# Optimization experiments

Measured on AMD Instinct MI355X. Metric: run time of the kernel, lower is better.

The kernel has to match this reference:

```python
import jax, jax.numpy as jnp
import numpy as np
import math

EPS = 1e-5
N_HEADS = 4


def _ln(x, g, b):
    mu = jnp.mean(x, axis=-1, keepdims=True)
    var = jnp.mean((x - mu) ** 2, axis=-1, keepdims=True)
    return (x - mu) * jax.lax.rsqrt(var + EPS) * g + b


def _eq_ln(s, v, g, b, vscale):
    # scalar LayerNorm + equivariant vector norm rescaling
    s = _ln(s, g, b)
    vn = jnp.sqrt(jnp.sum(v * v, axis=-1, keepdims=True))  # (B,N,C,1)
    v = v / (vn + EPS) * jnp.mean(vn, axis=-2, keepdims=True) * vscale[None, None, :, None]
    return s, v


def _block(s, v, pos, Wq, bq, Wk, bk, Wv, bv, Wo, bo, w_dist, b_dist, Wvv, Wvo,
           g1, be1, vs1, g2, be2, vs2, Wf1, bf1, Wf2, bf2, Wfv1, Wfv2):
    B, N, S = s.shape
    D = S // N_HEADS
    # --- norm1 + attention ---
    sn, vn = _eq_ln(s, v, g1, be1, vs1)
    q = (sn @ Wq + bq).reshape(B, N, N_HEADS, D)
    k = (sn @ Wk + bk).reshape(B, N, N_HEADS, D)
    vs = (sn @ Wv + bv).reshape(B, N, N_HEADS, D)
    attn = jnp.einsum('bnhd,bmhd->bhnm', q, k) / math.sqrt(D)
    # pairwise Euclidean distance via the |x|^2 + |y|^2 - 2xy trick (clamped for sqrt safety)
    p2 = jnp.sum(pos * pos, axis=-1)  # (B,N)
    d2 = p2[:, :, None] + p2[:, None, :] - 2.0 * jnp.einsum('bnd,bmd->bnm', pos, pos)
    dist = jnp.sqrt(jnp.maximum(d2, 1e-12))  # (B,N,N)
    # dist_proj: Linear(1 -> n_heads) + Softplus, applied per pair
    bias = jax.nn.softplus(dist[..., None] * w_dist + b_dist)  # (B,N,N,H)
    attn = jax.nn.softmax(attn - jnp.transpose(bias, (0, 3, 1, 2)), axis=-1)  # (B,H,N,N)
    attn_mean = jnp.mean(attn, axis=1)  # (B,N,N)
    s_attn = jnp.einsum('bhnm,bmhd->bnhd', attn, vs).reshape(B, N, S) @ Wo + bo
    # vector channel mixing + rotation by head-averaged attention
    v_mix = jnp.einsum('bncx,ce->bnex', vn, Wvv)          # (B,N,C,3)
    v_attn = jnp.einsum('bnm,bmcx->bncx', attn_mean, v_mix)
    v_attn = jnp.einsum('bncx,ce->bnex', v_attn, Wvo)
    s = s + s_attn
    v = v + v_attn
    # --- norm2 + FFN ---
    sn, vn = _eq_ln(s, v, g2, be2, vs2)
    s = s + (jax.nn.gelu(sn @ Wf1 + bf1, approximate=False) @ Wf2 + bf2)
    v = v + jnp.einsum('bnhx,hc->bncx', jnp.einsum('bncx,ch->bnhx', vn, Wfv1), Wfv2)
    return s, v


def setup_inputs() -> dict:
    B, N, S, C, H = 4, 2048, 256, 64, N_HEADS
    key = jax.random.key(0)
    ks = jax.random.split(key, 24)

    def nrm(k, shape, scale=0.02):
        return jax.random.normal(k, shape, dtype=jnp.float32) * scale

    return {
        's': jax.random.normal(ks[0], (B, N, S), dtype=jnp.float32),
        'v': jax.random.normal(ks[1], (B, N, C, 3), dtype=jnp.float32),
        'pos': jax.random.normal(ks[2], (B, N, 3), dtype=jnp.float32),
        'Wq': nrm(ks[3], (S, S)), 'bq': nrm(ks[4], (S,)),
        'Wk': nrm(ks[5], (S, S)), 'bk': nrm(ks[6], (S,)),
        'Wv': nrm(ks[7], (S, S)), 'bv': nrm(ks[8], (S,)),
        'Wo': nrm(ks[9], (S, S)), 'bo': nrm(ks[10], (S,)),
        'w_dist': nrm(ks[11], (H,), 0.5), 'b_dist': nrm(ks[12], (H,), 0.5),
        'Wvv': nrm(ks[13], (C, C)), 'Wvo': nrm(ks[14], (C, C)),
        'g1': jnp.ones((S,), jnp.float32), 'be1': jnp.zeros((S,), jnp.float32),
        'vs1': jnp.ones((C,), jnp.float32),
        'g2': jnp.ones((S,), jnp.float32), 'be2': jnp.zeros((S,), jnp.float32),
        'vs2': jnp.ones((C,), jnp.float32),
        'Wf1': nrm(ks[15], (S, 4 * S)), 'bf1': nrm(ks[16], (4 * S,)),
        'Wf2': nrm(ks[17], (4 * S, S)), 'bf2': nrm(ks[18], (S,)),
        'Wfv1': nrm(ks[19], (C, 4 * C)), 'Wfv2': nrm(ks[20], (4 * C, C)),
    }


def reference(s, v, pos, Wq, bq, Wk, bk, Wv, bv, Wo, bo, w_dist, b_dist, Wvv, Wvo,
              g1, be1, vs1, g2, be2, vs2, Wf1, bf1, Wf2, bf2, Wfv1, Wfv2):
    return _block(s, v, pos, Wq, bq, Wk, bk, Wv, bv, Wo, bo, w_dist, b_dist, Wvv, Wvo,
                  g1, be1, vs1, g2, be2, vs2, Wf1, bf1, Wf2, bf2, Wfv1, Wfv2)
```

## Files before the change

### kernel.cpp

```cpp
#include <hip/hip_runtime.h>
#include <hip/hip_bf16.h>

using bf16 = __hip_bfloat16;
typedef __attribute__((ext_vector_type(8))) short short8;
typedef __attribute__((ext_vector_type(4))) float float4v;
typedef __attribute__((ext_vector_type(16))) float f32x16;
typedef __attribute__((ext_vector_type(4))) unsigned uint4v;

__device__ __forceinline__ float b2f(bf16 x){ return __bfloat162float(x); }
__device__ __forceinline__ bf16  f2b(float x){ return __float2bfloat16(x); }
__device__ __forceinline__ bf16  tob(float x){ return f2b(x); }
__device__ __forceinline__ bf16  tob(bf16 x){ return x; }
__device__ __forceinline__ float frcp(float x){ return __builtin_amdgcn_rcpf(x); }
__device__ __forceinline__ float bs2f(short s){
  unsigned u = ((unsigned)(unsigned short)s) << 16;
  return __builtin_bit_cast(float, u);
}
__device__ __forceinline__ unsigned cvt_pk_bf16(float lo, float hi){
  unsigned r; asm("v_cvt_pk_bf16_f32 %0, %1, %2" : "=v"(r) : "v"(lo), "v"(hi)); return r;
}
__device__ __forceinline__ void plswap(unsigned &a, unsigned &b){
  asm("v_permlane32_swap_b32 %0, %1" : "+v"(a), "+v"(b));
}

#define EPSV 1e-5f
#define Z16 {0.f,0.f,0.f,0.f,0.f,0.f,0.f,0.f,0.f,0.f,0.f,0.f,0.f,0.f,0.f,0.f}

__global__ __launch_bounds__(256) void pos_kernel(const float* __restrict__ pos,
                                                  float* __restrict__ posf, int rows){
  int r = blockIdx.x*256 + threadIdx.x;
  if (r >= rows) return;
  float x = pos[3*r], y = pos[3*r+1], z = pos[3*r+2];
  posf[4*r] = x; posf[4*r+1] = y; posf[4*r+2] = z; posf[4*r+3] = x*x + y*y + z*z;
}

struct WTDesc { const float* src; bf16* dst; int rows, cols; };
struct WTPack { WTDesc d[10]; };

__global__ __launch_bounds__(256) void wtrans_kernel(WTPack p){
  WTDesc w = p.d[blockIdx.z];
  long r0 = (long)blockIdx.y*32, c0 = (long)blockIdx.x*32;
  if (r0 >= w.rows || c0 >= w.cols) return;
  __shared__ bf16 tile[32][33];
  int tx = threadIdx.x & 31, ty = threadIdx.x >> 5;
#pragma unroll
  for (int i = ty; i < 32; i += 8) tile[i][tx] = f2b(w.src[(r0+i)*w.cols + c0 + tx]);
  __syncthreads();
#pragma unroll
  for (int i = ty; i < 32; i += 8) w.dst[(c0+i)*w.rows + r0 + tx] = tile[tx][i];
}

template<typename TI>
__global__ __launch_bounds__(256) void transpose_kernel(
    const TI* __restrict__ in, long ldin, long is1, long is2,
    bf16* __restrict__ out, long ldout, long os1, long os2, int Z2)
{
  int z = blockIdx.z, z1 = z / Z2, z2 = z - z1*Z2;
  in  += (long)z1*is1 + (long)z2*is2;
  out += (long)z1*os1 + (long)z2*os2;
  __shared__ bf16 tile[32][33];
  int tx = threadIdx.x & 31, ty = threadIdx.x >> 5;
  long r0 = (long)blockIdx.y*32, c0 = (long)blockIdx.x*32;
#pragma unroll
  for (int i = ty; i < 32; i += 8) tile[i][tx] = tob(in[(r0+i)*ldin + c0 + tx]);
  __syncthreads();
#pragma unroll
  for (int i = ty; i < 32; i += 8) out[(c0+i)*ldout + r0 + tx] = tile[tx][i];
}

__global__ __launch_bounds__(256) void bcat_kernel(const float* __restrict__ bq,
                                                   const float* __restrict__ bk,
                                                   const float* __restrict__ bv,
                                                   float* __restrict__ bqkv,
                                                   float* __restrict__ kmax){
  int j = blockIdx.x*256 + threadIdx.x;
  if (blockIdx.x == 0 && threadIdx.x < 16) kmax[threadIdx.x] = 0.f;
  if (j >= 768) return;
  bqkv[j] = (j < 256) ? bq[j] : (j < 512) ? bk[j-256] : bv[j-512];
}

__global__ __launch_bounds__(256) void ln_kernel(const float* __restrict__ x,
                                                 const float* __restrict__ g,
                                                 const float* __restrict__ be,
                                                 bf16* __restrict__ out){
  const long row = blockIdx.x;
  const int t = threadIdx.x, lane = t & 63, wv = t >> 6;
  __shared__ float ws1[4], ws2[4];
  float v = x[(row<<8) + t];
  float s1 = v, s2 = v*v;
#pragma unroll
  for (int off=32; off; off>>=1){
    s1 += __shfl_xor(s1, off);
    s2 += __shfl_xor(s2, off);
  }
  if (lane == 0){ ws1[wv] = s1; ws2[wv] = s2; }
  __syncthreads();
  const float r1 = ws1[0]+ws1[1]+ws1[2]+ws1[3];
  const float r2 = ws2[0]+ws2[1]+ws2[2]+ws2[3];
  const float mu = r1 * (1.f/256.f);
  const float var = r2 * (1.f/256.f) - mu*mu;
  const float rstd = rsqrtf(fmaxf(var, 0.f) + EPSV);
  out[(row<<8)+t] = f2b((v-mu)*rstd*g[t] + be[t]);
}

__global__ __launch_bounds__(192) void vnorm1_kernel(const float* __restrict__ vin,
                                                     const float* __restrict__ vs1,
                                                     bf16* __restrict__ vnX){
  const long row = blockIdx.x;
  const int t = threadIdx.x;
  __shared__ float vv[192], nrm[64];
  __shared__ float smean;
  vv[t] = vin[row*192 + t];
  __syncthreads();
  if (t < 64){
    float a = vv[3*t], b = vv[3*t+1], c = vv[3*t+2];
    float nv = sqrtf(a*a + b*b + c*c);
    nrm[t] = nv;
    float s = nv;
#pragma unroll
    for (int off=32; off; off>>=1) s += __shfl_xor(s, off);
    if (t == 0) smean = s*(1.f/64.f);
  }
  __syncthreads();
  const int c = t/3, x = t - 3*c;
  const float val = vv[t] / (nrm[c] + EPSV) * smean * vs1[c];
  vnX[row*192 + x*64 + c] = f2b(val);
}

__global__ __launch_bounds__(192) void vnorm2_kernel(const float* __restrict__ v2X,
                                                     const float* __restrict__ vs2,
                                                     bf16* __restrict__ vn2X){
  const long row = blockIdx.x;
  const int t = threadIdx.x;
  __shared__ float vv[192], nrm[64];
  __shared__ float smean;
  vv[t] = v2X[row*192 + t];
  __syncthreads();
  if (t < 64){
    float a = vv[t], b = vv[t+64], c = vv[t+128];
    float nv = sqrtf(a*a + b*b + c*c);
    nrm[t] = nv;
    float s = nv;
#pragma unroll
    for (int off=32; off; off>>=1) s += __shfl_xor(s, off);
    if (t == 0) smean = s*(1.f/64.f);
  }
  __syncthreads();
  const int c = t & 63;
  vn2X[row*192 + t] = f2b(vv[t] / (nrm[c] + EPSV) * smean * vs2[c]);
}

__global__ __launch_bounds__(256) void knorm_kernel(const bf16* __restrict__ qkv,
                                                    float* __restrict__ kmax){
  const int bh = blockIdx.x, b = bh>>2, h = bh&3;
  const int t = threadIdx.x, lane = t & 63, wv = t >> 6;
  __shared__ float red[4];
  long row = (long)b*2048 + (long)blockIdx.y*256 + t;
  const short8* kp = (const short8*)(qkv + row*768 + 256 + h*64);
  float ss = 0.f;
#pragma unroll
  for (int c=0;c<8;c++){
    short8 v = kp[c];
#pragma unroll
    for (int j=0;j<8;j++){ float f = bs2f(v[j]); ss = fmaf(f,f,ss); }
  }
#pragma unroll
  for (int off=32; off; off>>=1) ss = fmaxf(ss, __shfl_xor(ss, off));
  if (lane == 0) red[wv] = ss;
  __syncthreads();
  if (t == 0){
    float m = fmaxf(fmaxf(red[0],red[1]), fmaxf(red[2],red[3]));
    atomicMax((unsigned*)&kmax[bh], __float_as_uint(m));
  }
}

#define ATT_K_OFF   0
#define ATT_V_OFF   4096
#define ATT_X_OFF   9216
#define ATT_P_OFF   24576
#define ATT_TILE    25088
#define ATT_GRP     50176
#define ATT_LACC    98304
#define ATT_SMEM    100352

__global__ __launch_bounds__(512, 2) void attn_kernel(
    const bf16* __restrict__ qkv,
    const bf16* __restrict__ vsT,
    const bf16* __restrict__ vmixT,
    const float* __restrict__ posf,
    const float* __restrict__ kmaxA,
    const float* __restrict__ w_dist, const float* __restrict__ b_dist,
    bf16* __restrict__ sA,
    bf16* __restrict__ slab)
{
  __shared__ __align__(16) char smem[ATT_SMEM];
  const int qb = blockIdx.x;
  const int bh = blockIdx.y;
  const int b  = bh >> 2, h = bh & 3;
  const int tid = threadIdx.x;
  const int w = tid >> 6, lane = tid & 63;
  const int g = w >> 2, qw = w & 3;
  const int lq = lane & 31, hi = lane >> 5;
  const int gtid = tid & 255;

  const int qloc = qb*128 + qw*32 + lq;
  const long rowQ = (long)b*2048 + qloc;

  short8 qf[4];
  {
    const bf16* qp = qkv + rowQ*768 + h*64 + hi*8;
#pragma unroll
    for (int kc=0;kc<4;kc++) qf[kc] = *(const short8*)(qp + kc*16);
  }
  float q2 = 0.f;
#pragma unroll
  for (int kc=0;kc<4;kc++)
#pragma unroll
    for (int j=0;j<8;j++){ float qv = bs2f(qf[kc][j]); q2 = fmaf(qv,qv,q2); }
  q2 += __shfl_xor(q2, 32);
  const float mxs = sqrtf(q2 * kmaxA[bh]) * 0.125f;
  const float wh = w_dist[h], bhd = b_dist[h];
  const float4v pn = *(const float4v*)(posf + (long)b*8192 + (long)qloc*4);
  const float m2x = -2.f*pn[0], m2y = -2.f*pn[1], m2z = -2.f*pn[2], pnw = pn[3];

  f32x16 O[2]  = {Z16, Z16};
  f32x16 VM[6] = {Z16, Z16, Z16, Z16, Z16, Z16};
  float lacc = 0.f;

  short8 stK, stV, stX0, stX1, stX2; float4v stP;
  const int sm = gtid >> 3, sc = gtid & 7;
  const int vd = gtid >> 2, vc = gtid & 3;
  const bf16* Kg = qkv + (long)b*2048*768 + 256 + h*64;
  const bf16* Vg = vsT + (long)b*524288 + (long)h*131072;
  const bf16* Xg = vmixT + (long)b*393216;
  const float* Pg = posf + (long)b*8192;
  char* gbase = smem + g*ATT_GRP;

  auto LOADT = [&](int m0){
    stK  = *(const short8*)(Kg + (long)(m0+sm)*768 + sc*8);
    stV  = *(const short8*)(Vg + (long)vd*2048 + m0 + vc*8);
    stX0 = *(const short8*)(Xg + (long)vd*2048 + m0 + vc*8);
    stX1 = *(const short8*)(Xg + (long)(64+vd)*2048 + m0 + vc*8);
    stX2 = *(const short8*)(Xg + (long)(128+vd)*2048 + m0 + vc*8);
    if (gtid < 32) stP = *(const float4v*)(Pg + (long)(m0+gtid)*4);
  };
  auto WRITET = [&](char* buf){
    *(short8*)(buf + ATT_K_OFF + sm*128 + ((sc ^ (sm&7))<<4)) = stK;
    *(short8*)(buf + ATT_V_OFF + vd*80 + vc*16) = stV;
    *(short8*)(buf + ATT_X_OFF + vd*80 + vc*16) = stX0;
    *(short8*)(buf + ATT_X_OFF + (64+vd)*80 + vc*16) = stX1;
    *(short8*)(buf + ATT_X_OFF + (128+vd)*80 + vc*16) = stX2;
    if (gtid < 32) *(float4v*)(buf + ATT_P_OFF + gtid*16) = stP;
  };

  auto COMPUTE = [&](const char* buf){
    const char* Kb = buf + ATT_K_OFF;
    const char* Vb = buf + ATT_V_OFF;
    const char* Xb = buf + ATT_X_OFF;
    const float4v* pmb = (const float4v*)(buf + ATT_P_OFF);
    f32x16 S = Z16;
#pragma unroll
    for (int kc=0;kc<4;kc++){
      short8 kf = *(const short8*)(Kb + lq*128 + (((kc*2+hi) ^ (lq&7))<<4));
      S = __builtin_amdgcn_mfma_f32_32x32x16_bf16(kf, qf[kc], S, 0, 0, 0);
    }
    float P[16];
#pragma unroll
    for (int gg=0; gg<4; gg++){
#pragma unroll
      for (int i=0;i<4;i++){
        float4v pm = pmb[gg*8 + hi*4 + i];
        float d2 = fmaf(m2x, pm[0], fmaf(m2y, pm[1], fmaf(m2z, pm[2], pnw + pm[3])));
        float dist = sqrtf(fmaxf(d2, 1e-12f));
        float sig = frcp(1.f + __expf(fmaf(dist, wh, bhd)));
        float p = __expf(fmaf(S[gg*4+i], 0.125f, -mxs)) * sig;
        lacc += p;
        P[gg*4+i] = p;
      }
    }
    unsigned pk[8];
#pragma unroll
    for (int t=0;t<8;t++) pk[t] = cvt_pk_bf16(P[2*t], P[2*t+1]);
    plswap(pk[0], pk[2]); plswap(pk[1], pk[3]);
    plswap(pk[4], pk[6]); plswap(pk[5], pk[7]);
    uint4v y0v = {pk[0], pk[1], pk[2], pk[3]};
    uint4v y1v = {pk[4], pk[5], pk[6], pk[7]};
    short8 Y0 = __builtin_bit_cast(short8, y0v);
    short8 Y1 = __builtin_bit_cast(short8, y1v);
#pragma unroll
    for (int dblk=0; dblk<2; dblk++){
      short8 v0 = *(const short8*)(Vb + (dblk*32+lq)*80 + hi*16);
      short8 v1 = *(const short8*)(Vb + (dblk*32+lq)*80 + 32 + hi*16);
      O[dblk] = __builtin_amdgcn_mfma_f32_32x32x16_bf16(v0, Y0, O[dblk], 0,0,0);
      O[dblk] = __builtin_amdgcn_mfma_f32_32x32x16_bf16(v1, Y1, O[dblk], 0,0,0);
    }
#pragma unroll
    for (int eblk=0; eblk<6; eblk++){
      short8 x0 = *(const short8*)(Xb + (eblk*32+lq)*80 + hi*16);
      short8 x1 = *(const short8*)(Xb + (eblk*32+lq)*80 + 32 + hi*16);
      VM[eblk] = __builtin_amdgcn_mfma_f32_32x32x16_bf16(x0, Y0, VM[eblk], 0,0,0);
      VM[eblk] = __builtin_amdgcn_mfma_f32_32x32x16_bf16(x1, Y1, VM[eblk], 0,0,0);
    }
  };

  LOADT(g*32);
  WRITET(gbase);
  __syncthreads();
#pragma unroll 1
  for (int i=0; i<32; ++i){
    if (i < 31) LOADT((2*(i+1)+g)*32);
    COMPUTE(gbase + (i&1)*ATT_TILE);
    if (i < 31) WRITET(gbase + ((i+1)&1)*ATT_TILE);
    __syncthreads();
  }

  float* laccT = (float*)(smem + ATT_LACC);
  laccT[w*64 + lane] = lacc;
  if (g == 1){
    float* Od = (float*)(smem + ATT_GRP) + (qw*64+lane)*33;
#pragma unroll
    for (int r=0;r<16;r++){ Od[r] = O[0][r]; Od[16+r] = O[1][r]; }
  }
  __syncthreads();
  const float lsum = laccT[qw*64+lq] + laccT[qw*64+32+lq]
                   + laccT[(4+qw)*64+lq] + laccT[(4+qw)*64+32+lq];
  if (g == 0){
    const float* Od = (const float*)(smem + ATT_GRP) + (qw*64+lane)*33;
#pragma unroll
    for (int r=0;r<16;r++){ O[0][r] += Od[r]; O[1][r] += Od[16+r]; }
  }
  __syncthreads();
#pragma unroll
  for (int hf=0; hf<2; hf++){
    if (g == 0){
      float* Vd = (float*)smem + (qw*64+lane)*49;
#pragma unroll
      for (int e=0;e<3;e++)
#pragma unroll
        for (int r=0;r<16;r++) Vd[e*16+r] = VM[hf*3+e][r];
    }
    __syncthreads();
    if (g == 1){
      const float* Vd = (const float*)smem + (qw*64+lane)*49;
#pragma unroll
      for (int e=0;e<3;e++)
#pragma unroll
        for (int r=0;r<16;r++) VM[hf*3+e][r] += Vd[e*16+r];
    }
    __syncthreads();
  }

  const float sinv = frcp(lsum);
  if (g == 0){
    char* scr = smem + qw*12544;
#pragma unroll
    for (int dblk=0; dblk<2; dblk++)
#pragma unroll
      for (int pp=0; pp<8; pp++){
        const int r = 2*pp;
        const int d = dblk*32 + (r&3) + 8*(r>>2) + 4*hi;
        unsigned u = cvt_pk_bf16(O[dblk][r]*sinv, O[dblk][r+1]*sinv);
        *(unsigned*)(scr + lq*136 + d*2) = u;
      }
  } else {
    const float vinv = 0.25f * sinv;
    char* scr = smem + ATT_GRP + qw*12544;
#pragma unroll
    for (int eblk=0; eblk<6; eblk++)
#pragma unroll
      for (int pp=0; pp<8; pp++){
        const int r = 2*pp;
        const int e = eblk*32 + (r&3) + 8*(r>>2) + 4*hi;
        unsigned u = cvt_pk_bf16(VM[eblk][r]*vinv, VM[eblk][r+1]*vinv);
        *(unsigned*)(scr + lq*392 + e*2) = u;
      }
  }
  __syncthreads();
  if (g == 0){
    const char* scr = smem + qw*12544;
    const int q = lane >> 1, half = lane & 1;
    const char* src = scr + q*136 + half*64;
    char* dst = (char*)(sA + (long)(b*2048 + qb*128 + qw*32 + q)*256 + h*64 + half*32);
#pragma unroll
    for (int i=0;i<8;i++)
      *(unsigned long long*)(dst + i*8) = *(const unsigned long long*)(src + i*8);
  } else {
    const char* scr = smem + ATT_GRP + qw*12544;
    const int q = lane >> 1, half = lane & 1;
    const char* src = scr + q*392 + half*192;
    char* dst = (char*)(slab + (long)h*1572864
                        + (long)(b*2048 + qb*128 + qw*32 + q)*192 + half*96);
#pragma unroll
    for (int i=0;i<24;i++)
      *(unsigned long long*)(dst + i*8) = *(const unsigned long long*)(src + i*8);
  }
}

__global__ __launch_bounds__(256) void hred_kernel(const bf16* __restrict__ slab,
                                                   bf16* __restrict__ out){
  long i = (long)blockIdx.x*256 + threadIdx.x;
  if (i >= 196608) return;
  const short8* s0 = (const short8*)slab + i;
  short8 a = s0[0], b = s0[196608], c = s0[2*196608], d = s0[3*196608];
  short8 o;
#pragma unroll
  for (int j=0;j<8;j++){
    float f = bs2f(a[j]) + bs2f(b[j]) + bs2f(c[j]) + bs2f(d[j]);
    bf16 hv = f2b(f); o[j] = *(short*)&hv;
  }
  ((short8*)out)[i] = o;
}

template<int ACT, int OUTM>
__global__ __launch_bounds__(256) void tgemm64_kernel(
    const bf16* __restrict__ A, long lda,
    const bf16* __restrict__ BT, long ldb,
    const float* __restrict__ bias,
    const float* __restrict__ resid,
    void* __restrict__ Cv, long ldc,
    int K)
{
  __shared__ __align__(16) bf16 As[2][64*32];
  __shared__ __align__(16) bf16 Bs[2][128*32];
  const int tid = threadIdx.x;
  const int wc = tid >> 6, lane = tid & 63;
  const int col = lane & 15, quad = lane >> 4;
  const long rowA0 = (long)blockIdx.y*64;
  const long colB0 = (long)blockIdx.x*128;

  const int tr = tid >> 2, tc = tid & 3;
  const bf16* Ag = A + (rowA0 + tr)*lda + tc*8;
  const bf16* Bg = BT + (colB0 + tr)*ldb + tc*8;

  short8 sa, sb[2];
  auto LOAD = [&](int k0){
    sa = *(const short8*)(Ag + k0);
    sb[0] = *(const short8*)(Bg + k0);
    sb[1] = *(const short8*)(Bg + (long)64*ldb + k0);
  };
  auto STORE = [&](int buf){
    *(short8*)(&As[buf][tr*32 + tc*8]) = sa;
    *(short8*)(&Bs[buf][tr*32 + tc*8]) = sb[0];
    *(short8*)(&Bs[buf][(tr+64)*32 + tc*8]) = sb[1];
  };

  float4v acc[4][2];
#pragma unroll
  for (int m=0;m<4;m++)
#pragma unroll
    for (int n=0;n<2;n++) acc[m][n] = (float4v){0.f,0.f,0.f,0.f};

  LOAD(0); STORE(0);
  __syncthreads();
  const int nk = K >> 5;
#pragma unroll 1
  for (int ks=0; ks<nk; ++ks){
    if (ks+1 < nk) LOAD((ks+1)*32);
    const bf16* Ab = &As[ks&1][col*32 + quad*8];
    const bf16* Bb = &Bs[ks&1][(wc*32 + col)*32 + quad*8];
    short8 af[4], bfv[2];
#pragma unroll
    for (int m=0;m<4;m++) af[m] = *(const short8*)(Ab + m*16*32);
#pragma unroll
    for (int n=0;n<2;n++) bfv[n] = *(const short8*)(Bb + n*16*32);
#pragma unroll
    for (int m=0;m<4;m++)
#pragma unroll
      for (int n=0;n<2;n++)
        acc[m][n] = __builtin_amdgcn_mfma_f32_16x16x32_bf16(af[m], bfv[n], acc[m][n], 0, 0, 0);
    if (ks+1 < nk) STORE((ks+1)&1);
    __syncthreads();
  }

#pragma unroll
  for (int m=0;m<4;m++){
    const long ci0 = rowA0 + m*16 + quad*4;
#pragma unroll
    for (int n=0;n<2;n++){
      const long cj = colB0 + wc*32 + n*16 + col;
      const float bbias = bias ? bias[cj] : 0.f;
#pragma unroll
      for (int r=0;r<4;r++){
        const long ci = ci0 + r;
        float val = acc[m][n][r] + bbias;
        if (ACT == 1) val = 0.5f*val*(1.f + erff(val*0.70710678118654752f));
        if (resid) val += resid[ci*ldc + cj];
        if (OUTM == 0) ((bf16*)Cv)[ci*ldc + cj] = f2b(val);
        else           ((float*)Cv)[ci*ldc + cj] = val;
      }
    }
  }
}

template<int MT, int NT, int ACT, int OUTM, int RXIL, int CXIL>
__global__ __launch_bounds__(64) void gemm_kernel(
    const bf16* __restrict__ A, long lda, long As1, long As2,
    const bf16* __restrict__ BT, long ldb, long Bs1, long Bs2,
    const float* __restrict__ bias,
    const float* __restrict__ resid, long ldr, long Rs1, long Rs2,
    void* __restrict__ Cv, long ldc, long Cs1, long Cs2,
    int K, int Z2, int KS)
{
  int z = blockIdx.z;
  int zz = z / KS, ks = z - zz*KS;
  int z1 = zz / Z2, z2 = zz - z1*Z2;
  A  += (long)z1*As1 + (long)z2*As2 + (long)ks*K;
  BT += (long)z1*Bs1 + (long)z2*Bs2 + (long)ks*K;
  if (resid) resid += (long)z1*Rs1 + (long)z2*Rs2;
  const long cbase = (long)z1*Cs1 + (long)z2*Cs2;

  const int lane = threadIdx.x;
  const int col = lane & 15, quad = lane >> 4;
  const long rowA0 = (long)blockIdx.y*(16*MT);
  const long colB0 = (long)blockIdx.x*(16*NT);

  float4v acc[MT][NT];
#pragma unroll
  for (int m=0;m<MT;m++)
#pragma unroll
    for (int n=0;n<NT;n++) acc[m][n] = (float4v){0.f,0.f,0.f,0.f};

  const bf16* ap[MT];
  const bf16* bp[NT];
#pragma unroll
  for (int m=0;m<MT;m++) ap[m] = A + (rowA0 + m*16 + col)*lda + quad*8;
#pragma unroll
  for (int n=0;n<NT;n++) bp[n] = BT + (colB0 + n*16 + col)*ldb + quad*8;

  for (int k0 = 0; k0 < K; k0 += 32){
    short8 a[MT], bb[NT];
#pragma unroll
    for (int m=0;m<MT;m++){ a[m] = *(const short8*)ap[m]; ap[m] += 32; }
#pragma unroll
    for (int n=0;n<NT;n++){ bb[n] = *(const short8*)bp[n]; bp[n] += 32; }
#pragma unroll
    for (int m=0;m<MT;m++)
#pragma unroll
      for (int n=0;n<NT;n++)
        acc[m][n] = __builtin_amdgcn_mfma_f32_16x16x32_bf16(a[m], bb[n], acc[m][n], 0, 0, 0);
  }

#pragma unroll
  for (int m=0;m<MT;m++){
    const long ri = rowA0 + m*16 + quad*4;
#pragma unroll
    for (int n=0;n<NT;n++){
      const long cj = colB0 + n*16 + col;
      const float bbias = bias ? bias[cj] : 0.f;
#pragma unroll
      for (int r=0;r<4;r++){
        const long ci = ri + r;
        float val = acc[m][n][r] + bbias;
        if (ACT == 1) val = 0.5f*val*(1.f + erff(val*0.70710678118654752f));
        if (resid){
          const long raddr = RXIL ? ((ci/3)*192 + cj*3 + (ci%3)) : (ci*ldr + cj);
          val += resid[raddr];
        }
        const long caddr = CXIL ? (cbase + (ci/3)*192 + cj*3 + (ci%3))
                                : (cbase + ci*ldc + cj);
        if (OUTM == 0)      ((bf16*)Cv)[caddr] = f2b(val);
        else if (OUTM == 1) ((float*)Cv)[caddr] = val;
        else                unsafeAtomicAdd(&((float*)Cv)[caddr], val);
      }
    }
  }
}

extern "C" void kernel_launch(void* const* d_in, const int* in_sizes, int n_in,
                              void* d_out, int out_size, void* d_ws, size_t ws_size,
                              hipStream_t stream)
{
  const float* s    = (const float*)d_in[0];
  const float* v    = (const float*)d_in[1];
  const float* pos  = (const float*)d_in[2];
  const float* Wq   = (const float*)d_in[3];
  const float* bq   = (const float*)d_in[4];
  const float* Wk   = (const float*)d_in[5];
  const float* bk   = (const float*)d_in[6];
  const float* Wv   = (const float*)d_in[7];
  const float* bv   = (const float*)d_in[8];
  const float* Wo   = (const float*)d_in[9];
  const float* bo   = (const float*)d_in[10];
  const float* w_d  = (const float*)d_in[11];
  const float* b_d  = (const float*)d_in[12];
  const float* Wvv  = (const float*)d_in[13];
  const float* Wvo  = (const float*)d_in[14];
  const float* g1   = (const float*)d_in[15];
  const float* be1  = (const float*)d_in[16];
  const float* vs1  = (const float*)d_in[17];
  const float* g2   = (const float*)d_in[18];
  const float* be2  = (const float*)d_in[19];
  const float* vs2  = (const float*)d_in[20];
  const float* Wf1  = (const float*)d_in[21];
  const float* bf1  = (const float*)d_in[22];
  const float* Wf2  = (const float*)d_in[23];
  const float* bf2  = (const float*)d_in[24];
  const float* Wfv1 = (const float*)d_in[25];
  const float* Wfv2 = (const float*)d_in[26];

  float* outS = (float*)d_out;
  float* outV = outS + (size_t)4*2048*256;

  char* w = (char*)d_ws;
  size_t o = 0;
  auto alloc = [&](size_t bytes)->char* {
    char* p = w + o;
    o = (o + bytes + 255) & ~(size_t)255;
    return p;
  };
  float* posf  = (float*)alloc(131072);
  bf16* WqkvT = (bf16*)alloc(393216);
  bf16* WoT   = (bf16*)alloc(131072);
  bf16* Wf1T  = (bf16*)alloc(524288);
  bf16* Wf2T  = (bf16*)alloc(524288);
  bf16* WvvT  = (bf16*)alloc(8192);
  bf16* WvoT  = (bf16*)alloc(8192);
  bf16* Wfv1T = (bf16*)alloc(32768);
  bf16* Wfv2T = (bf16*)alloc(32768);
  float* bqkv = (float*)alloc(3072);
  float* kmax = (float*)alloc(64);
  bf16* sn    = (bf16*)alloc(4194304);
  bf16* qkv   = (bf16*)alloc(12582912);
  bf16* vsT   = (bf16*)alloc(4194304);
  bf16* sA    = (bf16*)alloc(4194304);
  float* s2   = (float*)alloc(8388608);
  bf16* vnX   = (bf16*)alloc(3145728);
  bf16* vmixX = (bf16*)alloc(3145728);
  bf16* vmixXT= (bf16*)alloc(3145728);
  float* v2X  = (float*)alloc(6291456);
  bf16* slab  = (bf16*)alloc(12582912);
  bf16* h1    = (bf16*)alloc(16777216);
  bf16* vn2X  = vnX;
  bf16* tvXb  = vmixX;
  bf16* hv    = qkv;
  if (o > ws_size) return;

  pos_kernel<<<32, 256, 0, stream>>>(pos, posf, 8192);
  WTPack pk;
  pk.d[0] = {Wq,   WqkvT,          256, 256};
  pk.d[1] = {Wk,   WqkvT + 65536,  256, 256};
  pk.d[2] = {Wv,   WqkvT + 131072, 256, 256};
  pk.d[3] = {Wo,   WoT,            256, 256};
  pk.d[4] = {Wf1,  Wf1T,           256, 1024};
  pk.d[5] = {Wf2,  Wf2T,           1024, 256};
  pk.d[6] = {Wvv,  WvvT,           64, 64};
  pk.d[7] = {Wvo,  WvoT,           64, 64};
  pk.d[8] = {Wfv1, Wfv1T,          64, 256};
  pk.d[9] = {Wfv2, Wfv2T,          256, 64};
  wtrans_kernel<<<dim3(32,32,10), 256, 0, stream>>>(pk);
  bcat_kernel<<<3, 256, 0, stream>>>(bq, bk, bv, bqkv, kmax);

  ln_kernel<<<8192, 256, 0, stream>>>(s, g1, be1, sn);
  vnorm1_kernel<<<8192, 192, 0, stream>>>(v, vs1, vnX);

  gemm_kernel<2,4,0,0,0,0><<<dim3(1,768,1), 64, 0, stream>>>(vnX,64,0,0, WvvT,64,0,0,
      nullptr, nullptr,0,0,0, vmixX,64,0,0, 64, 1, 1);
  transpose_kernel<bf16><<<dim3(6,64,4), 256, 0, stream>>>(vmixX, 192, 393216,0,
      vmixXT, 2048, 393216,0, 1);

  tgemm64_kernel<0,0><<<dim3(6,128), 256, 0, stream>>>(sn,256, WqkvT,256,
      bqkv, nullptr, qkv,768, 256);
  transpose_kernel<bf16><<<dim3(2,64,16), 256, 0, stream>>>(qkv+512, 768, 1572864,64,
      vsT, 2048, 524288,131072, 4);

  knorm_kernel<<<dim3(16,8), 256, 0, stream>>>(qkv, kmax);
  attn_kernel<<<dim3(16,16), 512, 0, stream>>>(qkv, vsT, vmixXT, posf, kmax,
      w_d, b_d, sA, slab);
  hred_kernel<<<768, 256, 0, stream>>>(slab, tvXb);

  tgemm64_kernel<0,1><<<dim3(2,128), 256, 0, stream>>>(sA,256, WoT,256,
      bo, s, s2,256, 256);

  gemm_kernel<2,4,0,1,1,0><<<dim3(1,768,1), 64, 0, stream>>>(tvXb,64,0,0, WvoT,64,0,0,
      nullptr, v,0,0,0, v2X,64,0,0, 64, 1, 1);

  ln_kernel<<<8192, 256, 0, stream>>>(s2, g2, be2, sn);
  tgemm64_kernel<1,0><<<dim3(8,128), 256, 0, stream>>>(sn,256, Wf1T,256,
      bf1, nullptr, h1,1024, 256);
  tgemm64_kernel<0,1><<<dim3(2,128), 256, 0, stream>>>(h1,1024, Wf2T,1024,
      bf2, s2, outS,256, 1024);

  vnorm2_kernel<<<8192, 192, 0, stream>>>(v2X, vs2, vn2X);
  tgemm64_kernel<0,0><<<dim3(2,384), 256, 0, stream>>>(vn2X,64, Wfv1T,64,
      nullptr, nullptr, hv,256, 64);
  gemm_kernel<2,4,0,1,0,1><<<dim3(1,768,1), 64, 0, stream>>>(hv,256,0,0, Wfv2T,256,0,0,
      nullptr, v2X,64,0,0, outV,0,0,0, 256, 1, 1);
}
```

Baseline: 377.7 us.

## Merge small setup kernels, fuse head reduction, split-K output GEMMs with atomics

Folds pos and bias-concat into the weight-transpose launch, merges LN with vector-norm and the V transpose with the key-norm pass, and drops the hred kernel by summing the four head slabs inside the Wvo GEMM's A load. The Wo and Wf2 GEMMs become split-K over two z-slices that atomically add into an output pre-filled with residual plus bias by a new addb kernel. This cuts launch count and raises the block count for the small GEMMs. It adds atomic traffic, nondeterministic summation order, and extra passes over memory for the bias prefill.

```diff
diff --git a/kernel.cpp b/kernel.cpp
--- a/kernel.cpp
+++ b/kernel.cpp
@@ -26,23 +26,32 @@
 #define EPSV 1e-5f
 #define Z16 {0.f,0.f,0.f,0.f,0.f,0.f,0.f,0.f,0.f,0.f,0.f,0.f,0.f,0.f,0.f,0.f}
 
-__global__ __launch_bounds__(256) void pos_kernel(const float* __restrict__ pos,
-                                                  float* __restrict__ posf, int rows){
-  int r = blockIdx.x*256 + threadIdx.x;
-  if (r >= rows) return;
-  float x = pos[3*r], y = pos[3*r+1], z = pos[3*r+2];
-  posf[4*r] = x; posf[4*r+1] = y; posf[4*r+2] = z; posf[4*r+3] = x*x + y*y + z*z;
-}
-
 struct WTDesc { const float* src; bf16* dst; int rows, cols; };
 struct WTPack { WTDesc d[10]; };
 
-__global__ __launch_bounds__(256) void wtrans_kernel(WTPack p){
+__global__ __launch_bounds__(256) void wtrans_kernel(WTPack p,
+    const float* __restrict__ pos, float* __restrict__ posf,
+    const float* __restrict__ bq, const float* __restrict__ bk,
+    const float* __restrict__ bv, float* __restrict__ bqkv,
+    float* __restrict__ kmax){
+  const int t = threadIdx.x;
+  if (blockIdx.z == 10){
+    if (blockIdx.y == 0 && blockIdx.x < 32){
+      int r = blockIdx.x*256 + t;
+      float x = pos[3*r], y = pos[3*r+1], z = pos[3*r+2];
+      posf[4*r] = x; posf[4*r+1] = y; posf[4*r+2] = z; posf[4*r+3] = x*x + y*y + z*z;
+    } else if (blockIdx.y == 1 && blockIdx.x < 3){
+      int j = blockIdx.x*256 + t;
+      if (blockIdx.x == 0 && t < 16) kmax[t] = 0.f;
+      bqkv[j] = (j < 256) ? bq[j] : (j < 512) ? bk[j-256] : bv[j-512];
+    }
+    return;
+  }
   WTDesc w = p.d[blockIdx.z];
   long r0 = (long)blockIdx.y*32, c0 = (long)blockIdx.x*32;
   if (r0 >= w.rows || c0 >= w.cols) return;
   __shared__ bf16 tile[32][33];
-  int tx = threadIdx.x & 31, ty = threadIdx.x >> 5;
+  int tx = t & 31, ty = t >> 5;
 #pragma unroll
   for (int i = ty; i < 32; i += 8) tile[i][tx] = f2b(w.src[(r0+i)*w.cols + c0 + tx]);
   __syncthreads();
@@ -68,110 +77,110 @@
   for (int i = ty; i < 32; i += 8) out[(c0+i)*ldout + r0 + tx] = tile[tx][i];
 }
 
-__global__ __launch_bounds__(256) void bcat_kernel(const float* __restrict__ bq,
-                                                   const float* __restrict__ bk,
-                                                   const float* __restrict__ bv,
-                                                   float* __restrict__ bqkv,
-                                                   float* __restrict__ kmax){
-  int j = blockIdx.x*256 + threadIdx.x;
-  if (blockIdx.x == 0 && threadIdx.x < 16) kmax[threadIdx.x] = 0.f;
-  if (j >= 768) return;
-  bqkv[j] = (j < 256) ? bq[j] : (j < 512) ? bk[j-256] : bv[j-512];
-}
-
-__global__ __launch_bounds__(256) void ln_kernel(const float* __restrict__ x,
-                                                 const float* __restrict__ g,
-                                                 const float* __restrict__ be,
-                                                 bf16* __restrict__ out){
-  const long row = blockIdx.x;
-  const int t = threadIdx.x, lane = t & 63, wv = t >> 6;
-  __shared__ float ws1[4], ws2[4];
-  float v = x[(row<<8) + t];
-  float s1 = v, s2 = v*v;
-#pragma unroll
-  for (int off=32; off; off>>=1){
-    s1 += __shfl_xor(s1, off);
-    s2 += __shfl_xor(s2, off);
-  }
-  if (lane == 0){ ws1[wv] = s1; ws2[wv] = s2; }
-  __syncthreads();
-  const float r1 = ws1[0]+ws1[1]+ws1[2]+ws1[3];
-  const float r2 = ws2[0]+ws2[1]+ws2[2]+ws2[3];
-  const float mu = r1 * (1.f/256.f);
-  const float var = r2 * (1.f/256.f) - mu*mu;
-  const float rstd = rsqrtf(fmaxf(var, 0.f) + EPSV);
-  out[(row<<8)+t] = f2b((v-mu)*rstd*g[t] + be[t]);
-}
-
-__global__ __launch_bounds__(192) void vnorm1_kernel(const float* __restrict__ vin,
-                                                     const float* __restrict__ vs1,
-                                                     bf16* __restrict__ vnX){
-  const long row = blockIdx.x;
+__global__ __launch_bounds__(256) void trk_kernel(const bf16* __restrict__ qkv,
+                                                  bf16* __restrict__ vsT,
+                                                  float* __restrict__ kmax){
   const int t = threadIdx.x;
-  __shared__ float vv[192], nrm[64];
-  __shared__ float smean;
-  vv[t] = vin[row*192 + t];
-  __syncthreads();
-  if (t < 64){
-    float a = vv[3*t], b = vv[3*t+1], c = vv[3*t+2];
-    float nv = sqrtf(a*a + b*b + c*c);
-    nrm[t] = nv;
-    float s = nv;
-#pragma unroll
-    for (int off=32; off; off>>=1) s += __shfl_xor(s, off);
-    if (t == 0) smean = s*(1.f/64.f);
-  }
-  __syncthreads();
-  const int c = t/3, x = t - 3*c;
-  const float val = vv[t] / (nrm[c] + EPSV) * smean * vs1[c];
-  vnX[row*192 + x*64 + c] = f2b(val);
-}
-
-__global__ __launch_bounds__(192) void vnorm2_kernel(const float* __restrict__ v2X,
-                                                     const float* __restrict__ vs2,
-                                                     bf16* __restrict__ vn2X){
-  const long row = blockIdx.x;
+  if (blockIdx.z < 16){
+    int z = blockIdx.z, z1 = z >> 2, z2 = z & 3;
+    const bf16* in = qkv + 512 + (long)z1*1572864 + (long)z2*64;
+    bf16* out = vsT + (long)z1*524288 + (long)z2*131072;
+    __shared__ bf16 tile[32][33];
+    int tx = t & 31, ty = t >> 5;
+    long r0 = (long)blockIdx.y*32, c0 = (long)blockIdx.x*32;
+#pragma unroll
+    for (int i = ty; i < 32; i += 8) tile[i][tx] = in[(r0+i)*768 + c0 + tx];
+    __syncthreads();
+#pragma unroll
+    for (int i = ty; i < 32; i += 8) out[(c0+i)*2048 + r0 + tx] = tile[tx][i];
+  } else {
+    const int idx = blockIdx.y*2 + blockIdx.x;
+    const int bh = idx >> 3, chunk = idx & 7;
+    const int b = bh >> 2, h = bh & 3;
+    const int lane = t & 63, wv = t >> 6;
+    __shared__ float red[4];
+    long row = (long)b*2048 + (long)chunk*256 + t;
+    const short8* kp = (const short8*)(qkv + row*768 + 256 + h*64);
+    float ss = 0.f;
+#pragma unroll
+    for (int c=0;c<8;c++){
+      short8 v = kp[c];
+#pragma unroll
+      for (int j=0;j<8;j++){ float f = bs2f(v[j]); ss = fmaf(f,f,ss); }
+    }
+#pragma unroll
+    for (int off=32; off; off>>=1) ss = fmaxf(ss, __shfl_xor(ss, off));
+    if (lane == 0) red[wv] = ss;
+    __syncthreads();
+    if (t == 0){
+      float m = fmaxf(fmaxf(red[0],red[1]), fmaxf(red[2],red[3]));
+      atomicMax((unsigned*)&kmax[bh], __float_as_uint(m));
+    }
+  }
+}
+
+template<int VN>
+__global__ __launch_bounds__(256) void lnvn_kernel(
+    const float* __restrict__ x, const float* __restrict__ g,
+    const float* __restrict__ be, bf16* __restrict__ outln,
+    const float* __restrict__ vin, const float* __restrict__ vs,
+    bf16* __restrict__ outvn)
+{
   const int t = threadIdx.x;
-  __shared__ float vv[192], nrm[64];
-  __shared__ float smean;
-  vv[t] = v2X[row*192 + t];
-  __syncthreads();
-  if (t < 64){
-    float a = vv[t], b = vv[t+64], c = vv[t+128];
-    float nv = sqrtf(a*a + b*b + c*c);
-    nrm[t] = nv;
-    float s = nv;
-#pragma unroll
-    for (int off=32; off; off>>=1) s += __shfl_xor(s, off);
-    if (t == 0) smean = s*(1.f/64.f);
-  }
-  __syncthreads();
-  const int c = t & 63;
-  vn2X[row*192 + t] = f2b(vv[t] / (nrm[c] + EPSV) * smean * vs2[c]);
-}
-
-__global__ __launch_bounds__(256) void knorm_kernel(const bf16* __restrict__ qkv,
-                                                    float* __restrict__ kmax){
-  const int bh = blockIdx.x, b = bh>>2, h = bh&3;
-  const int t = threadIdx.x, lane = t & 63, wv = t >> 6;
-  __shared__ float red[4];
-  long row = (long)b*2048 + (long)blockIdx.y*256 + t;
-  const short8* kp = (const short8*)(qkv + row*768 + 256 + h*64);
-  float ss = 0.f;
-#pragma unroll
-  for (int c=0;c<8;c++){
-    short8 v = kp[c];
-#pragma unroll
-    for (int j=0;j<8;j++){ float f = bs2f(v[j]); ss = fmaf(f,f,ss); }
-  }
-#pragma unroll
-  for (int off=32; off; off>>=1) ss = fmaxf(ss, __shfl_xor(ss, off));
-  if (lane == 0) red[wv] = ss;
-  __syncthreads();
-  if (t == 0){
-    float m = fmaxf(fmaxf(red[0],red[1]), fmaxf(red[2],red[3]));
-    atomicMax((unsigned*)&kmax[bh], __float_as_uint(m));
-  }
+  if (blockIdx.x < 8192){
+    const long row = blockIdx.x;
+    const int lane = t & 63, wv = t >> 6;
+    __shared__ float ws1[4], ws2[4];
+    float v = x[(row<<8) + t];
+    float s1 = v, s2 = v*v;
+#pragma unroll
+    for (int off=32; off; off>>=1){
+      s1 += __shfl_xor(s1, off);
+      s2 += __shfl_xor(s2, off);
+    }
+    if (lane == 0){ ws1[wv] = s1; ws2[wv] = s2; }
+    __syncthreads();
+    const float r1 = ws1[0]+ws1[1]+ws1[2]+ws1[3];
+    const float r2 = ws2[0]+ws2[1]+ws2[2]+ws2[3];
+    const float mu = r1 * (1.f/256.f);
+    const float var = r2 * (1.f/256.f) - mu*mu;
+    const float rstd = rsqrtf(fmaxf(var, 0.f) + EPSV);
+    outln[(row<<8)+t] = f2b((v-mu)*rstd*g[t] + be[t]);
+  } else {
+    const long row = blockIdx.x - 8192;
+    __shared__ float vv[192], nrm[64];
+    __shared__ float smean;
+    if (t < 192) vv[t] = vin[row*192 + t];
+    __syncthreads();
+    if (t < 64){
+      float a, b, c;
+      if (VN == 1){ a = vv[3*t]; b = vv[3*t+1]; c = vv[3*t+2]; }
+      else        { a = vv[t]; b = vv[t+64]; c = vv[t+128]; }
+      float nv = sqrtf(a*a + b*b + c*c);
+      nrm[t] = nv;
+      float s = nv;
+#pragma unroll
+      for (int off=32; off; off>>=1) s += __shfl_xor(s, off);
+      if (t == 0) smean = s*(1.f/64.f);
+    }
+    __syncthreads();
+    if (t < 192){
+      if (VN == 1){
+        const int c = t/3, xx = t - 3*c;
+        outvn[row*192 + xx*64 + c] = f2b(vv[t] / (nrm[c] + EPSV) * smean * vs[c]);
+      } else {
+        const int c = t & 63;
+        outvn[row*192 + t] = f2b(vv[t] / (nrm[c] + EPSV) * smean * vs[c]);
+      }
+    }
+  }
+}
+
+__global__ __launch_bounds__(256) void addb_kernel(const float* __restrict__ in,
+                                                   const float* __restrict__ bias,
+                                                   float* __restrict__ out){
+  long i = (long)blockIdx.x*256 + threadIdx.x;
+  out[i] = in[i] + bias[threadIdx.x];
 }
 
 #define ATT_K_OFF   0
@@ -396,21 +405,6 @@
   }
 }
 
-__global__ __launch_bounds__(256) void hred_kernel(const bf16* __restrict__ slab,
-                                                   bf16* __restrict__ out){
-  long i = (long)blockIdx.x*256 + threadIdx.x;
-  if (i >= 196608) return;
-  const short8* s0 = (const short8*)slab + i;
-  short8 a = s0[0], b = s0[196608], c = s0[2*196608], d = s0[3*196608];
-  short8 o;
-#pragma unroll
-  for (int j=0;j<8;j++){
-    float f = bs2f(a[j]) + bs2f(b[j]) + bs2f(c[j]) + bs2f(d[j]);
-    bf16 hv = f2b(f); o[j] = *(short*)&hv;
-  }
-  ((short8*)out)[i] = o;
-}
-
 template<int ACT, int OUTM>
 __global__ __launch_bounds__(256) void tgemm64_kernel(
     const bf16* __restrict__ A, long lda,
@@ -427,10 +421,11 @@
   const int col = lane & 15, quad = lane >> 4;
   const long rowA0 = (long)blockIdx.y*64;
   const long colB0 = (long)blockIdx.x*128;
+  const long koff = (long)blockIdx.z*K;
 
   const int tr = tid >> 2, tc = tid & 3;
-  const bf16* Ag = A + (rowA0 + tr)*lda + tc*8;
-  const bf16* Bg = BT + (colB0 + tr)*ldb + tc*8;
+  const bf16* Ag = A + (rowA0 + tr)*lda + koff + tc*8;
+  const bf16* Bg = BT + (colB0 + tr)*ldb + koff + tc*8;
 
   short8 sa, sb[2];
   auto LOAD = [&](int k0){
@@ -485,14 +480,15 @@
         float val = acc[m][n][r] + bbias;
         if (ACT == 1) val = 0.5f*val*(1.f + erff(val*0.70710678118654752f));
         if (resid) val += resid[ci*ldc + cj];
-        if (OUTM == 0) ((bf16*)Cv)[ci*ldc + cj] = f2b(val);
-        else           ((float*)Cv)[ci*ldc + cj] = val;
+        if (OUTM == 0)      ((bf16*)Cv)[ci*ldc + cj] = f2b(val);
+        else if (OUTM == 1) ((float*)Cv)[ci*ldc + cj] = val;
+        else                unsafeAtomicAdd(&((float*)Cv)[ci*ldc + cj], val);
       }
     }
   }
 }
 
-template<int MT, int NT, int ACT, int OUTM, int RXIL, int CXIL>
+template<int MT, int NT, int ACT, int OUTM, int RXIL, int CXIL, int HS>
 __global__ __launch_bounds__(64) void gemm_kernel(
     const bf16* __restrict__ A, long lda, long As1, long As2,
     const bf16* __restrict__ BT, long ldb, long Bs1, long Bs2,
@@ -530,7 +526,24 @@
   for (int k0 = 0; k0 < K; k0 += 32){
     short8 a[MT], bb[NT];
 #pragma unroll
-    for (int m=0;m<MT;m++){ a[m] = *(const short8*)ap[m]; ap[m] += 32; }
+    for (int m=0;m<MT;m++){
+      if (HS){
+        short8 x0 = *(const short8*)ap[m];
+        short8 x1 = *(const short8*)(ap[m] + 1572864);
+        short8 x2 = *(const short8*)(ap[m] + 3145728);
+        short8 x3 = *(const short8*)(ap[m] + 4718592);
+        short8 r;
+#pragma unroll
+        for (int j=0;j<8;j++){
+          float f = bs2f(x0[j]) + bs2f(x1[j]) + bs2f(x2[j]) + bs2f(x3[j]);
+          bf16 hb = f2b(f); r[j] = *(short*)&hb;
+        }
+        a[m] = r;
+      } else {
+        a[m] = *(const short8*)ap[m];
+      }
+      ap[m] += 32;
+    }
 #pragma unroll
     for (int n=0;n<NT;n++){ bb[n] = *(const short8*)bp[n]; bp[n] += 32; }
 #pragma unroll
@@ -631,11 +644,9 @@
   bf16* slab  = (bf16*)alloc(12582912);
   bf16* h1    = (bf16*)alloc(16777216);
   bf16* vn2X  = vnX;
-  bf16* tvXb  = vmixX;
   bf16* hv    = qkv;
   if (o > ws_size) return;
 
-  pos_kernel<<<32, 256, 0, stream>>>(pos, posf, 8192);
   WTPack pk;
   pk.d[0] = {Wq,   WqkvT,          256, 256};
   pk.d[1] = {Wk,   WqkvT + 65536,  256, 256};
@@ -647,42 +658,40 @@
   pk.d[7] = {Wvo,  WvoT,           64, 64};
   pk.d[8] = {Wfv1, Wfv1T,          64, 256};
   pk.d[9] = {Wfv2, Wfv2T,          256, 64};
-  wtrans_kernel<<<dim3(32,32,10), 256, 0, stream>>>(pk);
-  bcat_kernel<<<3, 256, 0, stream>>>(bq, bk, bv, bqkv, kmax);
-
-  ln_kernel<<<8192, 256, 0, stream>>>(s, g1, be1, sn);
-  vnorm1_kernel<<<8192, 192, 0, stream>>>(v, vs1, vnX);
-
-  gemm_kernel<2,4,0,0,0,0><<<dim3(1,768,1), 64, 0, stream>>>(vnX,64,0,0, WvvT,64,0,0,
+  wtrans_kernel<<<dim3(32,32,11), 256, 0, stream>>>(pk, pos, posf, bq, bk, bv, bqkv, kmax);
+
+  lnvn_kernel<1><<<16384, 256, 0, stream>>>(s, g1, be1, sn, v, vs1, vnX);
+
+  gemm_kernel<2,4,0,0,0,0,0><<<dim3(1,768,1), 64, 0, stream>>>(vnX,64,0,0, WvvT,64,0,0,
       nullptr, nullptr,0,0,0, vmixX,64,0,0, 64, 1, 1);
   transpose_kernel<bf16><<<dim3(6,64,4), 256, 0, stream>>>(vmixX, 192, 393216,0,
       vmixXT, 2048, 393216,0, 1);
 
   tgemm64_kernel<0,0><<<dim3(6,128), 256, 0, stream>>>(sn,256, WqkvT,256,
       bqkv, nullptr, qkv,768, 256);
-  transpose_kernel<bf16><<<dim3(2,64,16), 256, 0, stream>>>(qkv+512, 768, 1572864,64,
-      vsT, 2048, 524288,131072, 4);
-
-  knorm_kernel<<<dim3(16,8), 256, 0, stream>>>(qkv, kmax);
+
+  trk_kernel<<<dim3(2,64,17), 256, 0, stream>>>(qkv, vsT, kmax);
+
   attn_kernel<<<dim3(16,16), 512, 0, stream>>>(qkv, vsT, vmixXT, posf, kmax,
       w_d, b_d, sA, slab);
-  hred_kernel<<<768, 256, 0, stream>>>(slab, tvXb);
-
-  tgemm64_kernel<0,1><<<dim3(2,128), 256, 0, stream>>>(sA,256, WoT,256,
-      bo, s, s2,256, 256);
-
-  gemm_kernel<2,4,0,1,1,0><<<dim3(1,768,1), 64, 0, stream>>>(tvXb,64,0,0, WvoT,64,0,0,
+
+  addb_kernel<<<8192, 256, 0, stream>>>(s, bo, s2);
+  tgemm64_kernel<0,2><<<dim3(2,128,2), 256, 0, stream>>>(sA,256, WoT,256,
+      nullptr, nullptr, s2,256, 128);
+
+  gemm_kernel<2,4,0,1,1,0,1><<<dim3(1,768,1), 64, 0, stream>>>(slab,64,0,0, WvoT,64,0,0,
       nullptr, v,0,0,0, v2X,64,0,0, 64, 1, 1);
 
-  ln_kernel<<<8192, 256, 0, stream>>>(s2, g2, be2, sn);
+  lnvn_kernel<2><<<16384, 256, 0, stream>>>(s2, g2, be2, sn, v2X, vs2, vn2X);
+
   tgemm64_kernel<1,0><<<dim3(8,128), 256, 0, stream>>>(sn,256, Wf1T,256,
       bf1, nullptr, h1,1024, 256);
-  tgemm64_kernel<0,1><<<dim3(2,128), 256, 0, stream>>>(h1,1024, Wf2T,1024,
-      bf2, s2, outS,256, 1024);
-
-  vnorm2_kernel<<<8192, 192, 0, stream>>>(v2X, vs2, vn2X);
+  addb_kernel<<<8192, 256, 0, stream>>>(s2, bf2, outS);
+  tgemm64_kernel<0,2><<<dim3(2,128,2), 256, 0, stream>>>(h1,1024, Wf2T,1024,
+      nullptr, nullptr, outS,256, 512);
+
   tgemm64_kernel<0,0><<<dim3(2,384), 256, 0, stream>>>(vn2X,64, Wfv1T,64,
       nullptr, nullptr, hv,256, 64);
-  gemm_kernel<2,4,0,1,0,1><<<dim3(1,768,1), 64, 0, stream>>>(hv,256,0,0, Wfv2T,256,0,0,
+  gemm_kernel<2,4,0,1,0,1,0><<<dim3(1,768,1), 64, 0, stream>>>(hv,256,0,0, Wfv2T,256,0,0,
       nullptr, v2X,64,0,0, outV,0,0,0, 256, 1, 1);
 }
```

Result: no change. 373.5 us (-1.1%).
